# Kernel optimization log

Hardware: AMD Instinct MI355X
Metric: run time of the kernel (lower is better)

## Reference

```python
import jax, jax.numpy as jnp
import numpy as np

T, B, E, H = 64, 64, 128, 256
N_ITEMS, N_DATA = 50000, 20000
EPS = 1e-8


def setup_inputs() -> dict:
    key = jax.random.key(0)
    ks = jax.random.split(key, 20)
    lengths = jnp.sort(jax.random.randint(ks[0], (B,), 1, T + 1))[::-1]
    lengths = lengths.at[0].set(T)  # pack_padded_sequence expects max length first
    x = jax.random.randint(ks[1], (T, B), 1, N_ITEMS)
    tmask = jnp.arange(T)[:, None] < lengths[None, :]
    x = jnp.where(tmask, x, 0)  # padding index 0
    s = 0.05
    emb_table = (jax.random.normal(ks[2], (N_ITEMS, E)) * s).at[0].set(0.0)  # padding_idx=0
    data_embeddings = jax.random.normal(ks[3], (N_DATA, E)) * s
    return {
        'x': x, 'lengths': lengths,
        'emb_table': emb_table, 'data_embeddings': data_embeddings,
        'W_ih': jax.random.normal(ks[4], (4 * H, E)) * s,
        'W_hh': jax.random.normal(ks[5], (4 * H, H)) * s,
        'b_ih': jax.random.normal(ks[6], (4 * H,)) * s,
        'b_hh': jax.random.normal(ks[7], (4 * H,)) * s,
        'Wq': jax.random.normal(ks[8], (H, H)) * s, 'bq': jax.random.normal(ks[9], (H,)) * s,
        'Wk': jax.random.normal(ks[10], (H, H)) * s, 'bk': jax.random.normal(ks[11], (H,)) * s,
        'Wv': jax.random.normal(ks[12], (H, H)) * s, 'bv': jax.random.normal(ks[13], (H,)) * s,
        'W_out': jax.random.normal(ks[14], (E, H)) * s, 'b_out': jax.random.normal(ks[15], (E,)) * s,
    }


def _forward(x, lengths, emb_table, data_embeddings, W_ih, W_hh, b_ih, b_hh,
             Wq, bq, Wk, bk, Wv, bv, W_out, b_out):
    t_len, b_sz = x.shape
    e_dim = emb_table.shape[1]
    h_dim = W_hh.shape[1]

    embs0 = emb_table[x]  # (T, B, E); dropout is identity in eval mode
    initial_embs = jax.lax.stop_gradient(embs0)  # .clone().detach() in original

    # PositionalEncoding: original slices by x.size(1) == batch dim (faithful quirk)
    pos = jnp.arange(b_sz, dtype=jnp.float32)[:, None]
    div = jnp.exp(jnp.arange(0, e_dim, 2, dtype=jnp.float32) * (-jnp.log(10000.0) / e_dim))
    enc = jnp.stack([jnp.sin(pos * div), jnp.cos(pos * div)], axis=-1).reshape(b_sz, e_dim)
    embs = embs0 + enc[None, :, :]  # broadcast over time

    # single-layer LSTM over time (gate order i, f, g, o)
    def step(carry, x_t):
        h, c = carry
        gates = x_t @ W_ih.T + h @ W_hh.T + (b_ih + b_hh)  # (B, 4H)
        i, f, g, o = jnp.split(gates, 4, axis=-1)
        c = jax.nn.sigmoid(f) * c + jax.nn.sigmoid(i) * jnp.tanh(g)
        h = jax.nn.sigmoid(o) * jnp.tanh(c)
        return (h, c), h

    h0 = jnp.zeros((b_sz, h_dim), embs.dtype)
    (_, _), lstm_out = jax.lax.scan(step, (h0, h0), embs)  # (T, B, H)

    # pack/pad round-trip zeroes outputs past each length (LSTM is causal)
    tmask = jnp.arange(t_len)[:, None] < lengths[None, :]  # (T, B)
    lstm_out = lstm_out * tmask[:, :, None]
    lstm_out = lstm_out.transpose(1, 0, 2)  # (B, T, H)

    padding_mask = jnp.sum(lstm_out, axis=-1) != 0  # (B, T)

    q = lstm_out @ Wq.T + bq
    k = lstm_out @ Wk.T + bk
    v = lstm_out @ Wv.T + bv
    score = jnp.einsum('bth,bsh->bts', q, k) / jnp.sqrt(jnp.float32(h_dim))
    score = jnp.where(padding_mask[:, None, :], score, -jnp.inf)
    attn = jax.nn.softmax(score, axis=2)
    weighted = jnp.einsum('bts,bsh->bth', attn, v)  # (B, T, H)
    attn_output = jnp.mean(weighted, axis=1) @ W_out.T + b_out  # (B, E)

    # kNN: fused normalize + matmul + argmin + gather over all T at once
    qn = initial_embs / jnp.clip(jnp.linalg.norm(initial_embs, axis=-1, keepdims=True), EPS)
    dn = data_embeddings / jnp.clip(jnp.linalg.norm(data_embeddings, axis=-1, keepdims=True), EPS)
    sims = jnp.einsum('tbe,ne->tbn', qn, dn)  # (T, B, N_DATA)
    idx = jnp.argmax(sims, axis=-1)  # argmin of (1 - sim)
    closest = jnp.mean(data_embeddings[idx], axis=0)  # (B, E)

    attn_output = attn_output * closest
    return attn_output @ emb_table.T  # (B, n_items)


def reference(x, lengths, emb_table, data_embeddings, W_ih, W_hh, b_ih, b_hh,
              Wq, bq, Wk, bk, Wv, bv, W_out, b_out):
    return _forward(x, lengths, emb_table, data_embeddings, W_ih, W_hh, b_ih, b_hh,
                    Wq, bq, Wk, bk, Wv, bv, W_out, b_out)
```

## Files before the change

kernel.cpp:

```cpp
#include <hip/hip_runtime.h>

typedef unsigned int uint;
typedef unsigned short ushort;
typedef unsigned long long u64;

#define NITEMS 50000
#define NDATA  20000
#define BLKCAP 4096u
#define OVCAP  65536u

#define OFF_LSTMOUT   0x0000000ULL
#define OFF_HX        0x0400000ULL
#define OFF_HXM       0x0440000ULL
#define OFF_PACKED    0x0480000ULL
#define OFF_PACKED2   0x0488000ULL
#define OFF_HITCNTS   0x0490000ULL
#define OFF_OHITCNT   0x0490800ULL
#define MEMSET_BYTES  0x0491000ULL
#define OFF_QMARGIN   0x0491000ULL
#define OFF_XW        0x05A0000ULL
#define OFF_QKV       0x15A0000ULL
#define OFF_HITBUF    OFF_QKV
#define OFF_WIHT      0x21A0000ULL
#define OFF_WQKVT     0x2220000ULL
#define OFF_BIASIH    0x22E0000ULL
#define OFF_BQKV      0x22E1000ULL
#define OFF_DNSCALE   0x22E2000ULL
#define OFF_CLOSEST   0x22F6000ULL
#define OFF_AV        0x22FE000ULL
#define OFF_DEMB16    0x2306000ULL
#define OFF_A16       0x27E8000ULL
#define OFF_OVF       0x28E8000ULL

__device__ __forceinline__ ushort f2bf(float f) {
  union { float f; uint u; } v; v.f = f;
  uint u = v.u;
  return (ushort)((u + 0x7FFFu + ((u >> 16) & 1u)) >> 16);
}
__device__ __forceinline__ uint fkey(float f) {
  union { float f; uint u; } v; v.f = f;
  return (v.u & 0x80000000u) ? ~v.u : (v.u | 0x80000000u);
}
__device__ __forceinline__ u64 shfl_xor_u64(u64 v, int off) {
  uint lo = (uint)v, hi = (uint)(v >> 32);
  lo = (uint)__shfl_xor((int)lo, off);
  hi = (uint)__shfl_xor((int)hi, off);
  return ((u64)hi << 32) | (u64)lo;
}

typedef __attribute__((ext_vector_type(8))) short short8;
typedef __attribute__((ext_vector_type(4))) float floatx4;

#define R32(M) M(0) M(1) M(2) M(3) M(4) M(5) M(6) M(7) M(8) M(9) M(10) M(11) \
  M(12) M(13) M(14) M(15) M(16) M(17) M(18) M(19) M(20) M(21) M(22) M(23) \
  M(24) M(25) M(26) M(27) M(28) M(29) M(30) M(31)

#define HIX(j) ((j) + (((j) >> 7) << 2))

#define LBAR() do { \
  __builtin_amdgcn_sched_barrier(0); \
  asm volatile("s_waitcnt lgkmcnt(0)" ::: "memory"); \
  __builtin_amdgcn_s_barrier(); \
  __builtin_amdgcn_sched_barrier(0); \
} while (0)

__global__ __launch_bounds__(256) void prep_kernel(
    const int* __restrict__ x,
    const float* __restrict__ emb, const float* __restrict__ demb,
    const float* __restrict__ W_ih,
    const float* __restrict__ Wq, const float* __restrict__ Wk, const float* __restrict__ Wv,
    const float* __restrict__ b_ih, const float* __restrict__ b_hh,
    const float* __restrict__ bq, const float* __restrict__ bk, const float* __restrict__ bv,
    float* __restrict__ dnscale, ushort* __restrict__ demb16, ushort* __restrict__ a16,
    float* __restrict__ wiht, float* __restrict__ wqkvt,
    float* __restrict__ biasih, float* __restrict__ bqkv,
    float* __restrict__ qmargin, u64* __restrict__ packed2)
{
  int blk = blockIdx.x, tid = threadIdx.x;
  if (blk < 5000) {
    int row = blk * 4 + (tid >> 6);
    int lane = tid & 63;
    float2 d = *(const float2*)(demb + (size_t)row * 128 + lane * 2);
    float s = d.x * d.x + d.y * d.y;
    for (int off = 32; off; off >>= 1) s += __shfl_xor(s, off);
    if (lane == 0) dnscale[row] = 1.0f / fmaxf(sqrtf(s), 1e-8f);
  } else if (blk < 6250) {
    size_t base = ((size_t)(blk - 5000) * 256 + tid) * 8;
    float4 f1 = *(const float4*)(demb + base);
    float4 f2 = *(const float4*)(demb + base + 4);
    uint4 o;
    o.x = (uint)f2bf(f1.x) | ((uint)f2bf(f1.y) << 16);
    o.y = (uint)f2bf(f1.z) | ((uint)f2bf(f1.w) << 16);
    o.z = (uint)f2bf(f2.x) | ((uint)f2bf(f2.y) << 16);
    o.w = (uint)f2bf(f2.z) | ((uint)f2bf(f2.w) << 16);
    *(uint4*)(demb16 + base) = o;
  } else if (blk < 6506) {
    int idx = (blk - 6250) * 256 + tid;
    int m = idx >> 4, seg = idx & 15;
    const float* src = emb + (size_t)x[m] * 128 + seg * 8;
    float4 f1 = *(const float4*)(src);
    float4 f2 = *(const float4*)(src + 4);
    uint4 o;
    o.x = (uint)f2bf(f1.x) | ((uint)f2bf(f1.y) << 16);
    o.y = (uint)f2bf(f1.z) | ((uint)f2bf(f1.w) << 16);
    o.z = (uint)f2bf(f2.x) | ((uint)f2bf(f2.y) << 16);
    o.w = (uint)f2bf(f2.z) | ((uint)f2bf(f2.w) << 16);
    *(uint4*)(a16 + (size_t)m * 128 + seg * 8) = o;
  } else if (blk < 7018) {
    int f = (blk - 6506) * 256 + tid;
    int r = f >> 7, e = f & 127;
    wiht[e * 1024 + r] = W_ih[f];
  } else if (blk < 7786) {
    int f = (blk - 7018) * 256 + tid;
    int w = f >> 16; int rem = f & 65535;
    int r = rem >> 8, e = rem & 255;
    const float* src = (w == 0) ? Wq : (w == 1) ? Wk : Wv;
    wqkvt[e * 768 + w * 256 + r] = src[rem];
  } else if (blk < 7790) {
    int idx = (blk - 7786) * 256 + tid;
    if (idx < 1024) biasih[idx] = b_ih[idx] + b_hh[idx];
  } else if (blk < 7793) {
    int idx = (blk - 7790) * 256 + tid;
    if (idx < 768) {
      int w = idx >> 8; int r = idx & 255;
      const float* src = (w == 0) ? bq : (w == 1) ? bk : bv;
      bqkv[idx] = src[r];
    }
  } else {
    int row = (blk - 7793) * 4 + (tid >> 6);
    int lane = tid & 63;
    float2 d = *(const float2*)(emb + (size_t)x[row] * 128 + lane * 2);
    float s = d.x * d.x + d.y * d.y;
    for (int off = 32; off; off >>= 1) s += __shfl_xor(s, off);
    if (lane == 0) {
      if (s == 0.f) {
        qmargin[row] = -1e30f;
        packed2[row] = ((u64)fkey(0.0f) << 32) | 0xFFFFFFFFull;
      } else {
        qmargin[row] = 0.017f * sqrtf(s) + 1e-5f;
      }
    }
  }
}

__global__ __launch_bounds__(256) void xw_kernel(
    const int* __restrict__ x, const float* __restrict__ emb,
    const float* __restrict__ wiht, const float* __restrict__ biasih,
    float* __restrict__ xW)
{
  __shared__ __align__(16) float At[128 * 16];
  int blk = blockIdx.x, tid = threadIdx.x;
  int m0 = blk * 16;
  for (int c = 0; c < 8; ++c) {
    int idx = c * 256 + tid;
    int mm = idx >> 7, e = idx & 127;
    int m = m0 + mm;
    int bcol = m & 63;
    int xv = x[m];
    float val = emb[(size_t)xv * 128 + e];
    int j = e >> 1;
    float arg = (float)bcol * __expf((float)j * -0.14391157f);
    val += (e & 1) ? cosf(arg) : sinf(arg);
    At[e * 16 + mm] = val;
  }
  __syncthreads();
  int quad = tid >> 6, l = tid & 63;
  for (int rp = 0; rp < 4; ++rp) {
    int r = rp * 256 + l * 4;
    float acc[4][4] = {};
    for (int e = 0; e < 128; ++e) {
      float4 wv4 = *(const float4*)(wiht + e * 1024 + r);
      float4 av4 = *(const float4*)(At + e * 16 + quad * 4);
      float am[4] = {av4.x, av4.y, av4.z, av4.w};
      float wr4[4] = {wv4.x, wv4.y, wv4.z, wv4.w};
      #pragma unroll
      for (int mi = 0; mi < 4; ++mi)
        #pragma unroll
        for (int ri = 0; ri < 4; ++ri)
          acc[mi][ri] += am[mi] * wr4[ri];
    }
    float4 bv4 = *(const float4*)(biasih + r);
    #pragma unroll
    for (int mi = 0; mi < 4; ++mi) {
      size_t m = (size_t)(m0 + quad * 4 + mi);
      float4 o;
      o.x = acc[mi][0] + bv4.x; o.y = acc[mi][1] + bv4.y;
      o.z = acc[mi][2] + bv4.z; o.w = acc[mi][3] + bv4.w;
      *(float4*)(xW + m * 1024 + r) = o;
    }
  }
}

__global__ __launch_bounds__(256) void knn_kernel(
    const ushort* __restrict__ a16, const ushort* __restrict__ demb16,
    const float* __restrict__ dnscale, const float* __restrict__ qmargin,
    u64* __restrict__ packed, uint* __restrict__ hitcnts, uint* __restrict__ ohitcnt,
    uint* __restrict__ hitbuf, uint* __restrict__ ovbuf,
    const int* __restrict__ x, const float* __restrict__ emb,
    const float* __restrict__ demb, u64* __restrict__ packed2)
{
  __shared__ __align__(16) ushort b_sh[2][64 * 144];
  __shared__ uint lcnt;
  int blk = blockIdx.x, tid = threadIdx.x;
  int chunk = blk & 15, mt = blk >> 4;
  int wv = tid >> 6, lane = tid & 63;
  int col = lane & 15, quad = lane >> 4;
  int M0 = mt * 128;
  if (tid == 0) lcnt = 0;
  short8 afrag[2][4];
  #pragma unroll
  for (int s = 0; s < 2; ++s) {
    int mrow = M0 + s * 64 + wv * 16 + col;
    #pragma unroll
    for (int kf = 0; kf < 4; ++kf)
      afrag[s][kf] = *(const short8*)(a16 + (size_t)mrow * 128 + kf * 32 + quad * 8);
  }
  float best[2][4] = {{-1e30f,-1e30f,-1e30f,-1e30f},{-1e30f,-1e30f,-1e30f,-1e30f}};
  int bidx[2][4] = {};
  int nbase = chunk * 1250, nend = nbase + 1250;
  const int niter = 20;
  int srow = tid >> 4, sseg = tid & 15;
  uint4 stg[4]; float scr[4];

  #pragma unroll
  for (int p = 0; p < 4; ++p) {
    int n = nbase + p * 16 + srow;
    uint4 v = {0u,0u,0u,0u};
    if (n < nend) v = *(const uint4*)(demb16 + (size_t)n * 128 + sseg * 8);
    stg[p] = v;
  }
  #pragma unroll
  for (int ns = 0; ns < 4; ++ns) {
    int n = nbase + ns * 16 + col;
    scr[ns] = (n < nend) ? dnscale[n] : 0.f;
  }
  for (int it = 0; it < niter; ++it) {
    int n0 = nbase + it * 64;
    ushort* bsh = b_sh[it & 1];
    #pragma unroll
    for (int p = 0; p < 4; ++p)
      *(uint4*)(&bsh[(p * 16 + srow) * 144 + sseg * 8]) = stg[p];
    float mysc[4] = {scr[0], scr[1], scr[2], scr[3]};
    __syncthreads();
    if (it + 1 < niter) {
      int nb = n0 + 64;
      #pragma unroll
      for (int p = 0; p < 4; ++p) {
        int n = nb + p * 16 + srow;
        uint4 v = {0u,0u,0u,0u};
        if (n < nend) v = *(const uint4*)(demb16 + (size_t)n * 128 + sseg * 8);
        stg[p] = v;
      }
      #pragma unroll
      for (int ns = 0; ns < 4; ++ns) {
        int n = nb + ns * 16 + col;
        scr[ns] = (n < nend) ? dnscale[n] : 0.f;
      }
    }
    #pragma unroll
    for (int ns = 0; ns < 4; ++ns) {
      short8 bfr[4];
      #pragma unroll
      for (int kf = 0; kf < 4; ++kf)
        bfr[kf] = *(const short8*)(&bsh[(ns * 16 + col) * 144 + kf * 32 + quad * 8]);
      int n = n0 + ns * 16 + col;
      float sc = mysc[ns];
      bool valid = (n < nend);
      #pragma unroll
      for (int s = 0; s < 2; ++s) {
        floatx4 acc = {0.f, 0.f, 0.f, 0.f};
        #pragma unroll
        for (int kf = 0; kf < 4; ++kf)
          acc = __builtin_amdgcn_mfma_f32_16x16x32_bf16(afrag[s][kf], bfr[kf], acc, 0, 0, 0);
        #pragma unroll
        for (int r = 0; r < 4; ++r) {
          float sim = acc[r] * sc;
          if (valid && sim > best[s][r]) { best[s][r] = sim; bidx[s][r] = n; }
        }
      }
    }
  }
  float thr[2][4];
  #pragma unroll
  for (int s = 0; s < 2; ++s)
    #pragma unroll
    for (int r = 0; r < 4; ++r) {
      u64 p = ((u64)fkey(best[s][r]) << 32) | (u64)(0xFFFFFFFFu - (uint)bidx[s][r]);
      #pragma unroll
      for (int off = 1; off < 16; off <<= 1) {
        u64 o = shfl_xor_u64(p, off);
        if (o > p) p = o;
      }
      int m = M0 + s * 64 + wv * 16 + quad * 4 + r;
      union { uint u; float f; } bu;
      uint k = (uint)(p >> 32);
      bu.u = (k & 0x80000000u) ? (k & 0x7FFFFFFFu) : ~k;
      thr[s][r] = bu.f - qmargin[m];
      if (col == 0)
        atomicMax((unsigned long long*)&packed[m], (unsigned long long)p);
    }
  __syncthreads();

  uint* myregion = hitbuf + (size_t)blk * BLKCAP;
  uint* ovregion = ovbuf;
  #pragma unroll
  for (int p = 0; p < 4; ++p) {
    int n = nbase + p * 16 + srow;
    uint4 v = {0u,0u,0u,0u};
    if (n < nend) v = *(const uint4*)(demb16 + (size_t)n * 128 + sseg * 8);
    stg[p] = v;
  }
  #pragma unroll
  for (int ns = 0; ns < 4; ++ns) {
    int n = nbase + ns * 16 + col;
    scr[ns] = (n < nend) ? dnscale[n] : 0.f;
  }
  for (int it = 0; it < niter; ++it) {
    int n0 = nbase + it * 64;
    ushort* bsh = b_sh[it & 1];
    #pragma unroll
    for (int p = 0; p < 4; ++p)
      *(uint4*)(&bsh[(p * 16 + srow) * 144 + sseg * 8]) = stg[p];
    float mysc[4] = {scr[0], scr[1], scr[2], scr[3]};
    __syncthreads();
    if (it + 1 < niter) {
      int nb = n0 + 64;
      #pragma unroll
      for (int p = 0; p < 4; ++p) {
        int n = nb + p * 16 + srow;
        uint4 v = {0u,0u,0u,0u};
        if (n < nend) v = *(const uint4*)(demb16 + (size_t)n * 128 + sseg * 8);
        stg[p] = v;
      }
      #pragma unroll
      for (int ns = 0; ns < 4; ++ns) {
        int n = nb + ns * 16 + col;
        scr[ns] = (n < nend) ? dnscale[n] : 0.f;
      }
    }
    #pragma unroll
    for (int ns = 0; ns < 4; ++ns) {
      short8 bfr[4];
      #pragma unroll
      for (int kf = 0; kf < 4; ++kf)
        bfr[kf] = *(const short8*)(&bsh[(ns * 16 + col) * 144 + kf * 32 + quad * 8]);
      int n = n0 + ns * 16 + col;
      float sc = mysc[ns];
      bool valid = (n < nend);
      #pragma unroll
      for (int s = 0; s < 2; ++s) {
        floatx4 acc = {0.f, 0.f, 0.f, 0.f};
        #pragma unroll
        for (int kf = 0; kf < 4; ++kf)
          acc = __builtin_amdgcn_mfma_f32_16x16x32_bf16(afrag[s][kf], bfr[kf], acc, 0, 0, 0);
        #pragma unroll
        for (int r = 0; r < 4; ++r) {
          float sim = acc[r] * sc;
          bool hit = valid && (sim >= thr[s][r]);
          u64 mask = __ballot(hit);
          if (mask) {
            uint lcntv = (uint)__popcll(mask);
            int leader = __ffsll((unsigned long long)mask) - 1;
            uint base = 0;
            if (lane == leader) base = atomicAdd(&lcnt, lcntv);
            base = (uint)__shfl((int)base, leader);
            if (hit) {
              uint pos = base + (uint)__popcll(mask & ((1ull << lane) - 1ull));
              uint mm = (uint)(M0 + s * 64 + wv * 16 + quad * 4 + r);
              uint rec = (mm << 15) | (uint)n;
              if (pos < BLKCAP) {
                myregion[pos] = rec;
              } else {
                uint op = atomicAdd(ohitcnt, 1u);
                if (op < OVCAP) ovregion[op] = rec;
              }
            }
          }
        }
      }
    }
  }
  __syncthreads();
  if (tid == 0) hitcnts[blk] = lcnt;
  uint rcnt = lcnt; if (rcnt > BLKCAP) rcnt = BLKCAP;
  for (uint h = tid; h < rcnt; h += 256) {
    uint rec = myregion[h];
    uint m = rec >> 15, n = rec & 0x7FFFu;
    if (m >= 4096 || n >= NDATA) continue;
    const float* qr = emb + (size_t)x[m] * 128;
    const float* dr = demb + (size_t)n * 128;
    double p = 0.0;
    #pragma unroll 8
    for (int e = 0; e < 128; e += 2) {
      float2 qv = *(const float2*)(qr + e);
      float2 dv = *(const float2*)(dr + e);
      p += (double)qv.x * (double)dv.x + (double)qv.y * (double)dv.y;
    }
    float sx = (float)(p * (double)dnscale[n]);
    u64 key = ((u64)fkey(sx) << 32) | (u64)(0xFFFFFFFFu - n);
    atomicMax((unsigned long long*)&packed2[m], (unsigned long long)key);
  }
}

__global__ __launch_bounds__(512, 2) void lstm_kernel(
    const int* __restrict__ lengths, const float* __restrict__ Whh,
    const float* __restrict__ xW, float* __restrict__ lstm_out,
    u64* __restrict__ hx, u64* __restrict__ hxm)
{
  __shared__ __align__(16) float h_sh[264];
  __shared__ float part_sh[256];
  int blk = blockIdx.x, tid = threadIdx.x;
  int b = blk & 63, q = blk >> 6;
  int row_local = tid >> 1, half = tid & 1;
  int gate = row_local >> 6, jloc = row_local & 63;
  int grow = gate * 256 + q * 64 + jloc;
  const float4* wp4 = (const float4*)(Whh + (size_t)grow * 256 + half * 128);
#define WDECL(i) float4 tt##i = wp4[i]; \
  float w##i##x = tt##i.x, w##i##y = tt##i.y, w##i##z = tt##i.z, w##i##w = tt##i.w;
  R32(WDECL)
#define WPIN(i) asm volatile("" : "+v"(w##i##x), "+v"(w##i##y), "+v"(w##i##z), "+v"(w##i##w));
  R32(WPIN)
  int len = lengths[b];
  if (tid < 256) h_sh[HIX(tid)] = 0.f;
  float cval = 0.f;
  int prm = tid - 320;
  int jr = (prm < q * 64) ? prm : prm + 64;
  bool fast_ok = true;
  int j1 = q * 64 + (tid - 64);
  float xw0 = 0.f, xw1 = 0.f, xw2 = 0.f, xw3 = 0.f;
  if (tid < 64) {
    const float* xwrow = xW + ((size_t)0 * 64 + b) * 1024 + q * 64 + tid;
    xw0 = xwrow[0]; xw1 = xwrow[256]; xw2 = xwrow[512]; xw3 = xwrow[768];
  }
  __syncthreads();
  for (int t = 0; t < len; ++t) {
    float nx0 = 0.f, nx1 = 0.f, nx2 = 0.f, nx3 = 0.f;
    if (tid < 64 && t + 1 < len) {
      const float* xwrow = xW + ((size_t)(t + 1) * 64 + b) * 1024 + q * 64 + tid;
      nx0 = xwrow[0]; nx1 = xwrow[256]; nx2 = xwrow[512]; nx3 = xwrow[768];
    }
    float hprev = 0.f;
    if (tid >= 64 && tid < 128 && t > 0) hprev = h_sh[HIX(j1)];
    const float4* h4 = (const float4*)(h_sh + half * 132);
    float a[4] = {0.f, 0.f, 0.f, 0.f};
#define WACC(i) { float4 hv_ = h4[i]; \
    a[(i) & 3] += w##i##x * hv_.x + w##i##y * hv_.y + w##i##z * hv_.z + w##i##w * hv_.w; }
    R32(WACC)
    float acc = (a[0] + a[2]) + (a[1] + a[3]);
    acc += __shfl_xor(acc, 1);
    if (!half) part_sh[row_local] = acc;
    LBAR();
    if (tid < 64) {
      float gi = part_sh[tid]       + xw0;
      float gf = part_sh[64 + tid]  + xw1;
      float gg = part_sh[128 + tid] + xw2;
      float go = part_sh[192 + tid] + xw3;
      float ii = 1.f / (1.f + __expf(-gi));
      float ff = 1.f / (1.f + __expf(-gf));
      float oo = 1.f / (1.f + __expf(-go));
      float tg = 1.f - 2.f / (1.f + __expf(2.f * gg));
      cval = ff * cval + ii * tg;
      float tc = 1.f - 2.f / (1.f + __expf(2.f * cval));
      float hv = oo * tc;
      int j = q * 64 + tid;
      union { float f; uint u; } cu; cu.f = hv;
      u64 pk = ((u64)cu.u << 32) | (u64)(uint)(t + 1);
      size_t slot = ((size_t)((t + 1) & 1) * 64 + b) * 256 + j;
      __builtin_amdgcn_sched_barrier(0);
      asm volatile("s_waitcnt vmcnt(4)" ::: "memory");
      asm volatile("global_store_dwordx2 %0, %1, off"
                   :: "v"(hxm + slot), "v"(pk) : "memory");
      __hip_atomic_store(hx + slot, pk, __ATOMIC_RELAXED, __HIP_MEMORY_SCOPE_AGENT);
      h_sh[HIX(j)] = hv;
      xw0 = nx0; xw1 = nx1; xw2 = nx2; xw3 = nx3;
    } else if (tid < 128) {
      if (t > 0) lstm_out[((size_t)b * 64 + (t - 1)) * 256 + j1] = hprev;
    } else if (tid >= 320 && t + 1 < len) {
      size_t slot = ((size_t)((t + 1) & 1) * 64 + b) * 256 + jr;
      uint want = (uint)(t + 1);
      u64 v = 0;
      bool got = false;
      if (fast_ok) {
        const u64* ms = hxm + slot;
        for (int tries = 0; tries < 32; ++tries) {
          asm volatile("global_load_dwordx2 %0, %1, off sc0\n\t"
                       "s_waitcnt vmcnt(0)"
                       : "=&v"(v) : "v"(ms) : "memory");
          if ((uint)v == want) { got = true; break; }
        }
        if (!got && t > 0) fast_ok = false;
      }
      if (!got) {
        const u64* as = hx + slot;
        int guard = 0;
        while (true) {
          v = __hip_atomic_load(as, __ATOMIC_RELAXED, __HIP_MEMORY_SCOPE_AGENT);
          if ((uint)v == want || ++guard > (1 << 24)) break;
        }
      }
      union { uint u; float f; } cv; cv.u = (uint)(v >> 32);
      h_sh[HIX(jr)] = cv.f;
    }
    LBAR();
  }
  if (tid >= 64 && tid < 128) {
    float hl = h_sh[HIX(j1)];
    lstm_out[((size_t)b * 64 + (len - 1)) * 256 + j1] = hl;
  }
}

__global__ __launch_bounds__(256) void fused_post_kernel(
    const float* __restrict__ lstm_out, const float* __restrict__ wqkvt,
    const float* __restrict__ bqkv, float* __restrict__ qkv,
    const u64* __restrict__ packed, const uint* __restrict__ ohitcnt,
    const uint* __restrict__ ovbuf, const int* __restrict__ x,
    const float* __restrict__ emb, const float* __restrict__ demb,
    const float* __restrict__ dnscale, u64* __restrict__ packed2)
{
  __shared__ __align__(16) float At[256 * 16];
  int blk = blockIdx.x, tid = threadIdx.x;
  if (blk < 256) {
    int m0 = blk * 16;
    for (int c = 0; c < 16; ++c)
      At[tid * 16 + c] = lstm_out[((size_t)m0 + c) * 256 + tid];
    __syncthreads();
    int quad = tid >> 6, l = tid & 63;
    for (int rp = 0; rp < 3; ++rp) {
      int r = rp * 256 + l * 4;
      float acc[4][4] = {};
      for (int e = 0; e < 256; ++e) {
        float4 wv4 = *(const float4*)(wqkvt + (size_t)e * 768 + r);
        float4 av4 = *(const float4*)(At + e * 16 + quad * 4);
        float am[4] = {av4.x, av4.y, av4.z, av4.w};
        float wr4[4] = {wv4.x, wv4.y, wv4.z, wv4.w};
        #pragma unroll
        for (int mi = 0; mi < 4; ++mi)
          #pragma unroll
          for (int ri = 0; ri < 4; ++ri)
            acc[mi][ri] += am[mi] * wr4[ri];
      }
      float4 bv4 = *(const float4*)(bqkv + r);
      #pragma unroll
      for (int mi = 0; mi < 4; ++mi) {
        size_t m = (size_t)(m0 + quad * 4 + mi);
        float4 o;
        o.x = acc[mi][0] + bv4.x; o.y = acc[mi][1] + bv4.y;
        o.z = acc[mi][2] + bv4.z; o.w = acc[mi][3] + bv4.w;
        *(float4*)(qkv + m * 768 + r) = o;
      }
    }
    return;
  }
  if (blk < 272) {
    uint m = (uint)(blk - 256) * 256 + tid;
    uint n = 0xFFFFFFFFu - (uint)(packed[m] & 0xFFFFFFFFull);
    if (n < NDATA) {
      const float* qr = emb + (size_t)x[m] * 128;
      const float* dr = demb + (size_t)n * 128;
      double p = 0.0;
      #pragma unroll 8
      for (int e = 0; e < 128; e += 2) {
        float2 qv = *(const float2*)(qr + e);
        float2 dv = *(const float2*)(dr + e);
        p += (double)qv.x * (double)dv.x + (double)qv.y * (double)dv.y;
      }
      float sx = (float)(p * (double)dnscale[n]);
      u64 key = ((u64)fkey(sx) << 32) | (u64)(0xFFFFFFFFu - n);
      atomicMax((unsigned long long*)&packed2[m], (unsigned long long)key);
    }
    return;
  }
  uint cnt = *ohitcnt; if (cnt > OVCAP) cnt = OVCAP;
  for (uint h = (uint)(blk - 272) * 256 + tid; h < cnt; h += 16 * 256) {
    uint rec = ovbuf[h];
    uint m = rec >> 15, n = rec & 0x7FFFu;
    if (m >= 4096 || n >= NDATA) continue;
    const float* qr = emb + (size_t)x[m] * 128;
    const float* dr = demb + (size_t)n * 128;
    double p = 0.0;
    #pragma unroll 8
    for (int e = 0; e < 128; e += 2) {
      float2 qv = *(const float2*)(qr + e);
      float2 dv = *(const float2*)(dr + e);
      p += (double)qv.x * (double)dv.x + (double)qv.y * (double)dv.y;
    }
    float sx = (float)(p * (double)dnscale[n]);
    u64 key = ((u64)fkey(sx) << 32) | (u64)(0xFFFFFFFFu - n);
    atomicMax((unsigned long long*)&packed2[m], (unsigned long long)key);
  }
}

__global__ __launch_bounds__(128) void closest_kernel(
    const u64* __restrict__ packed2, const float* __restrict__ demb,
    float* __restrict__ closest)
{
  int b = blockIdx.x, tid = threadIdx.x;
  float s = 0.f;
  for (int t = 0; t < 64; ++t) {
    uint low = (uint)(packed2[t * 64 + b] & 0xFFFFFFFFull);
    uint n = 0xFFFFFFFFu - low;
    if (n >= NDATA) n = 0;
    s += demb[(size_t)n * 128 + tid];
  }
  closest[b * 128 + tid] = s * (1.0f / 64.0f);
}

__global__ __launch_bounds__(256) void attn_kernel(
    const float* __restrict__ qkv, const int* __restrict__ lengths,
    const float* __restrict__ closest, const float* __restrict__ W_out,
    const float* __restrict__ b_out, float* __restrict__ av)
{
  __shared__ float k_sh[64 * 257];
  __shared__ __align__(16) float q_sh[4 * 256];
  __shared__ float wpart[4 * 64];
  __shared__ float wtot[64];
  __shared__ float out_sh[256];
  int b = blockIdx.x, tid = threadIdx.x;
  int wv = tid >> 6, lane = tid & 63;
  int len = lengths[b];
  for (int s = 0; s < 64; ++s)
    k_sh[s * 257 + tid] = qkv[((size_t)b * 64 + s) * 768 + 256 + tid];
  wpart[tid] = 0.f;
  for (int tq = 0; tq < 16; ++tq) {
    __syncthreads();
    #pragma unroll
    for (int c = 0; c < 4; ++c)
      q_sh[c * 256 + tid] = qkv[((size_t)b * 64 + tq * 4 + c) * 768 + tid];
    __syncthreads();
    const float* krow = k_sh + lane * 257;
    const float* qrow = q_sh + wv * 256;
    float sc = 0.f;
    #pragma unroll 8
    for (int h = 0; h < 256; ++h)
      sc += qrow[h] * krow[h];
    sc *= 0.0625f;
    bool vs = (lane < len);
    float scm = vs ? sc : -1e30f;
    float mx = scm;
    for (int off = 32; off; off >>= 1) mx = fmaxf(mx, __shfl_xor(mx, off));
    float e = vs ? __expf(sc - mx) : 0.f;
    float sum = e;
    for (int off = 32; off; off >>= 1) sum += __shfl_xor(sum, off);
    wpart[wv * 64 + lane] += e / sum;
  }
  __syncthreads();
  if (tid < 64)
    wtot[tid] = (wpart[tid] + wpart[64 + tid] + wpart[128 + tid] + wpart[192 + tid]) * (1.0f / 64.0f);
  __syncthreads();
  {
    float acc = 0.f;
    for (int s = 0; s < 64; ++s)
      acc += wtot[s] * qkv[((size_t)b * 64 + s) * 768 + 512 + tid];
    out_sh[tid] = acc;
  }
  __syncthreads();
  if (tid < 128) {
    const float4* wr = (const float4*)(W_out + (size_t)tid * 256);
    float p = b_out[tid];
    #pragma unroll
    for (int c = 0; c < 64; ++c) {
      float4 u = wr[c];
      p += out_sh[c * 4 + 0] * u.x + out_sh[c * 4 + 1] * u.y
         + out_sh[c * 4 + 2] * u.z + out_sh[c * 4 + 3] * u.w;
    }
    av[tid * 64 + b] = p * closest[b * 128 + tid];
  }
}

__global__ __launch_bounds__(256) void final_kernel(
    const float* __restrict__ emb, const float* __restrict__ av,
    float* __restrict__ out)
{
  int i = blockIdx.x * 256 + threadIdx.x;
  if (i >= NITEMS) return;
  const float4* row = (const float4*)(emb + (size_t)i * 128);
  float acc[64];
  #pragma unroll
  for (int bb = 0; bb < 64; ++bb) acc[bb] = 0.f;
  for (int e4 = 0; e4 < 32; ++e4) {
    float4 u = row[e4];
    float wvv[4] = {u.x, u.y, u.z, u.w};
    const float* ab = av + e4 * 4 * 64;
    #pragma unroll
    for (int j = 0; j < 4; ++j) {
      #pragma unroll
      for (int bb = 0; bb < 64; ++bb)
        acc[bb] += wvv[j] * ab[j * 64 + bb];
    }
  }
  #pragma unroll
  for (int bb = 0; bb < 64; ++bb)
    out[(size_t)bb * NITEMS + i] = acc[bb];
}

extern "C" void kernel_launch(void* const* d_in, const int* in_sizes, int n_in,
                              void* d_out, int out_size, void* d_ws, size_t ws_size,
                              hipStream_t stream)
{
  const int*   x       = (const int*)d_in[0];
  const int*   lengths = (const int*)d_in[1];
  const float* emb     = (const float*)d_in[2];
  const float* demb    = (const float*)d_in[3];
  const float* W_ih    = (const float*)d_in[4];
  const float* W_hh    = (const float*)d_in[5];
  const float* b_ih    = (const float*)d_in[6];
  const float* b_hh    = (const float*)d_in[7];
  const float* Wq      = (const float*)d_in[8];
  const float* bq      = (const float*)d_in[9];
  const float* Wk      = (const float*)d_in[10];
  const float* bk      = (const float*)d_in[11];
  const float* Wv      = (const float*)d_in[12];
  const float* bv      = (const float*)d_in[13];
  const float* W_out   = (const float*)d_in[14];
  const float* b_out   = (const float*)d_in[15];

  char* ws = (char*)d_ws;
  float*  lstm_out = (float*)(ws + OFF_LSTMOUT);
  u64*    hx       = (u64*)(ws + OFF_HX);
  u64*    hxm      = (u64*)(ws + OFF_HXM);
  u64*    packed   = (u64*)(ws + OFF_PACKED);
  u64*    packed2  = (u64*)(ws + OFF_PACKED2);
  uint*   hitcnts  = (uint*)(ws + OFF_HITCNTS);
  uint*   ohitcnt  = (uint*)(ws + OFF_OHITCNT);
  float*  qmargin  = (float*)(ws + OFF_QMARGIN);
  uint*   hitbuf   = (uint*)(ws + OFF_HITBUF);
  uint*   ovbuf    = (uint*)(ws + OFF_OVF);
  float*  xW       = (float*)(ws + OFF_XW);
  float*  qkv      = (float*)(ws + OFF_QKV);
  float*  wiht     = (float*)(ws + OFF_WIHT);
  float*  wqkvt    = (float*)(ws + OFF_WQKVT);
  float*  biasih   = (float*)(ws + OFF_BIASIH);
  float*  bqkv     = (float*)(ws + OFF_BQKV);
  float*  dnscale  = (float*)(ws + OFF_DNSCALE);
  float*  closest  = (float*)(ws + OFF_CLOSEST);
  float*  av       = (float*)(ws + OFF_AV);
  ushort* demb16   = (ushort*)(ws + OFF_DEMB16);
  ushort* a16      = (ushort*)(ws + OFF_A16);

  hipMemsetAsync(d_ws, 0, (size_t)MEMSET_BYTES, stream);

  hipLaunchKernelGGL(prep_kernel, dim3(8817), dim3(256), 0, stream,
                     x, emb, demb, W_ih, Wq, Wk, Wv, b_ih, b_hh, bq, bk, bv,
                     dnscale, demb16, a16, wiht, wqkvt, biasih, bqkv,
                     qmargin, packed2);
  hipLaunchKernelGGL(xw_kernel, dim3(256), dim3(256), 0, stream,
                     x, emb, wiht, biasih, xW);
  hipLaunchKernelGGL(knn_kernel, dim3(512), dim3(256), 0, stream,
                     a16, demb16, dnscale, qmargin, packed, hitcnts, ohitcnt,
                     hitbuf, ovbuf, x, emb, demb, packed2);
  hipLaunchKernelGGL(lstm_kernel, dim3(256), dim3(512), 0, stream,
                     lengths, W_hh, xW, lstm_out, hx, hxm);
  hipLaunchKernelGGL(fused_post_kernel, dim3(288), dim3(256), 0, stream,
                     lstm_out, wqkvt, bqkv, qkv, packed, ohitcnt, ovbuf,
                     x, emb, demb, dnscale, packed2);
  hipLaunchKernelGGL(closest_kernel, dim3(64), dim3(128), 0, stream,
                     packed2, demb, closest);
  hipLaunchKernelGGL(attn_kernel, dim3(64), dim3(256), 0, stream,
                     qkv, lengths, closest, W_out, b_out, av);
  hipLaunchKernelGGL(final_kernel, dim3(196), dim3(256), 0, stream,
                     emb, av, (float*)d_out);
}
```

Baseline: 584.8 us.

## Merge LSTM and kNN into one launch and fold closest into attention

Combines the latency-bound LSTM recurrence (256 blocks) and the kNN MFMA search (now 512-thread blocks, one 64-row slice per wave group) into a single 768-block launch. The kNN work can then run on compute units the serial LSTM leaves idle. The separate closest_kernel is also removed and its gather-mean is computed inside attn_kernel, saving one launch and a round trip through global memory. The risks are that the LSTM blocks rely on cross-block spin-waiting, so they must all be resident at once, and that kNN blocks competing with them for CUs may slow the critical recurrence.

```diff
diff --git a/kernel.cpp b/kernel.cpp
--- a/kernel.cpp
+++ b/kernel.cpp
@@ -26,7 +26,6 @@
 #define OFF_BIASIH    0x22E0000ULL
 #define OFF_BQKV      0x22E1000ULL
 #define OFF_DNSCALE   0x22E2000ULL
-#define OFF_CLOSEST   0x22F6000ULL
 #define OFF_AV        0x22FE000ULL
 #define OFF_DEMB16    0x2306000ULL
 #define OFF_A16       0x27E8000ULL
@@ -191,7 +190,10 @@
   }
 }
 
-__global__ __launch_bounds__(256) void knn_kernel(
+__global__ __launch_bounds__(512, 2) void lstm_knn_kernel(
+    const int* __restrict__ lengths, const float* __restrict__ Whh,
+    const float* __restrict__ xW, float* __restrict__ lstm_out,
+    u64* __restrict__ hx, u64* __restrict__ hxm,
     const ushort* __restrict__ a16, const ushort* __restrict__ demb16,
     const float* __restrict__ dnscale, const float* __restrict__ qmargin,
     u64* __restrict__ packed, uint* __restrict__ hitcnts, uint* __restrict__ ohitcnt,
@@ -199,32 +201,139 @@
     const int* __restrict__ x, const float* __restrict__ emb,
     const float* __restrict__ demb, u64* __restrict__ packed2)
 {
+  __shared__ __align__(16) float h_sh[264];
+  __shared__ float part_sh[256];
   __shared__ __align__(16) ushort b_sh[2][64 * 144];
   __shared__ uint lcnt;
-  int blk = blockIdx.x, tid = threadIdx.x;
-  int chunk = blk & 15, mt = blk >> 4;
-  int wv = tid >> 6, lane = tid & 63;
+  int tid = threadIdx.x;
+
+  if (blockIdx.x < 256) {
+    int blk = blockIdx.x;
+    int b = blk & 63, q = blk >> 6;
+    int row_local = tid >> 1, half = tid & 1;
+    int gate = row_local >> 6, jloc = row_local & 63;
+    int grow = gate * 256 + q * 64 + jloc;
+    const float4* wp4 = (const float4*)(Whh + (size_t)grow * 256 + half * 128);
+#define WDECL(i) float4 tt##i = wp4[i]; \
+  float w##i##x = tt##i.x, w##i##y = tt##i.y, w##i##z = tt##i.z, w##i##w = tt##i.w;
+    R32(WDECL)
+#define WPIN(i) asm volatile("" : "+v"(w##i##x), "+v"(w##i##y), "+v"(w##i##z), "+v"(w##i##w));
+    R32(WPIN)
+    int len = lengths[b];
+    if (tid < 256) h_sh[HIX(tid)] = 0.f;
+    float cval = 0.f;
+    int prm = tid - 320;
+    int jr = (prm < q * 64) ? prm : prm + 64;
+    bool fast_ok = true;
+    int j1 = q * 64 + (tid - 64);
+    float xw0 = 0.f, xw1 = 0.f, xw2 = 0.f, xw3 = 0.f;
+    if (tid < 64) {
+      const float* xwrow = xW + ((size_t)0 * 64 + b) * 1024 + q * 64 + tid;
+      xw0 = xwrow[0]; xw1 = xwrow[256]; xw2 = xwrow[512]; xw3 = xwrow[768];
+    }
+    __syncthreads();
+    for (int t = 0; t < len; ++t) {
+      float nx0 = 0.f, nx1 = 0.f, nx2 = 0.f, nx3 = 0.f;
+      if (tid < 64 && t + 1 < len) {
+        const float* xwrow = xW + ((size_t)(t + 1) * 64 + b) * 1024 + q * 64 + tid;
+        nx0 = xwrow[0]; nx1 = xwrow[256]; nx2 = xwrow[512]; nx3 = xwrow[768];
+      }
+      float hprev = 0.f;
+      if (tid >= 64 && tid < 128 && t > 0) hprev = h_sh[HIX(j1)];
+      const float4* h4 = (const float4*)(h_sh + half * 132);
+      float a[4] = {0.f, 0.f, 0.f, 0.f};
+#define WACC(i) { float4 hv_ = h4[i]; \
+    a[(i) & 3] += w##i##x * hv_.x + w##i##y * hv_.y + w##i##z * hv_.z + w##i##w * hv_.w; }
+      R32(WACC)
+      float acc = (a[0] + a[2]) + (a[1] + a[3]);
+      acc += __shfl_xor(acc, 1);
+      if (!half) part_sh[row_local] = acc;
+      LBAR();
+      if (tid < 64) {
+        float gi = part_sh[tid]       + xw0;
+        float gf = part_sh[64 + tid]  + xw1;
+        float gg = part_sh[128 + tid] + xw2;
+        float go = part_sh[192 + tid] + xw3;
+        float ii = 1.f / (1.f + __expf(-gi));
+        float ff = 1.f / (1.f + __expf(-gf));
+        float oo = 1.f / (1.f + __expf(-go));
+        float tg = 1.f - 2.f / (1.f + __expf(2.f * gg));
+        cval = ff * cval + ii * tg;
+        float tc = 1.f - 2.f / (1.f + __expf(2.f * cval));
+        float hv = oo * tc;
+        int j = q * 64 + tid;
+        union { float f; uint u; } cu; cu.f = hv;
+        u64 pk = ((u64)cu.u << 32) | (u64)(uint)(t + 1);
+        size_t slot = ((size_t)((t + 1) & 1) * 64 + b) * 256 + j;
+        __builtin_amdgcn_sched_barrier(0);
+        asm volatile("s_waitcnt vmcnt(4)" ::: "memory");
+        asm volatile("global_store_dwordx2 %0, %1, off"
+                     :: "v"(hxm + slot), "v"(pk) : "memory");
+        __hip_atomic_store(hx + slot, pk, __ATOMIC_RELAXED, __HIP_MEMORY_SCOPE_AGENT);
+        h_sh[HIX(j)] = hv;
+        xw0 = nx0; xw1 = nx1; xw2 = nx2; xw3 = nx3;
+      } else if (tid < 128) {
+        if (t > 0) lstm_out[((size_t)b * 64 + (t - 1)) * 256 + j1] = hprev;
+      } else if (tid >= 320 && t + 1 < len) {
+        size_t slot = ((size_t)((t + 1) & 1) * 64 + b) * 256 + jr;
+        uint want = (uint)(t + 1);
+        u64 v = 0;
+        bool got = false;
+        if (fast_ok) {
+          const u64* ms = hxm + slot;
+          for (int tries = 0; tries < 32; ++tries) {
+            asm volatile("global_load_dwordx2 %0, %1, off sc0\n\t"
+                         "s_waitcnt vmcnt(0)"
+                         : "=&v"(v) : "v"(ms) : "memory");
+            if ((uint)v == want) { got = true; break; }
+          }
+          if (!got && t > 0) fast_ok = false;
+        }
+        if (!got) {
+          const u64* as = hx + slot;
+          int guard = 0;
+          while (true) {
+            v = __hip_atomic_load(as, __ATOMIC_RELAXED, __HIP_MEMORY_SCOPE_AGENT);
+            if ((uint)v == want || ++guard > (1 << 24)) break;
+          }
+        }
+        union { uint u; float f; } cv; cv.u = (uint)(v >> 32);
+        h_sh[HIX(jr)] = cv.f;
+      }
+      LBAR();
+    }
+    if (tid >= 64 && tid < 128) {
+      float hl = h_sh[HIX(j1)];
+      lstm_out[((size_t)b * 64 + (len - 1)) * 256 + j1] = hl;
+    }
+    return;
+  }
+
+  int kb = blockIdx.x - 256;
+  int chunk = kb & 15, mt = kb >> 4;
+  int w8 = tid >> 6;
+  int s = w8 >> 2, wv2 = w8 & 3;
+  int lane = tid & 63;
   int col = lane & 15, quad = lane >> 4;
   int M0 = mt * 128;
   if (tid == 0) lcnt = 0;
-  short8 afrag[2][4];
-  #pragma unroll
-  for (int s = 0; s < 2; ++s) {
-    int mrow = M0 + s * 64 + wv * 16 + col;
+  short8 afrag[4];
+  {
+    int mrow = M0 + s * 64 + wv2 * 16 + col;
     #pragma unroll
     for (int kf = 0; kf < 4; ++kf)
-      afrag[s][kf] = *(const short8*)(a16 + (size_t)mrow * 128 + kf * 32 + quad * 8);
-  }
-  float best[2][4] = {{-1e30f,-1e30f,-1e30f,-1e30f},{-1e30f,-1e30f,-1e30f,-1e30f}};
-  int bidx[2][4] = {};
+      afrag[kf] = *(const short8*)(a16 + (size_t)mrow * 128 + kf * 32 + quad * 8);
+  }
+  float best[4] = {-1e30f, -1e30f, -1e30f, -1e30f};
+  int bidx[4] = {};
   int nbase = chunk * 1250, nend = nbase + 1250;
   const int niter = 20;
   int srow = tid >> 4, sseg = tid & 15;
-  uint4 stg[4]; float scr[4];
+  uint4 stg[2]; float scr[4];
 
   #pragma unroll
-  for (int p = 0; p < 4; ++p) {
-    int n = nbase + p * 16 + srow;
+  for (int p = 0; p < 2; ++p) {
+    int n = nbase + p * 32 + srow;
     uint4 v = {0u,0u,0u,0u};
     if (n < nend) v = *(const uint4*)(demb16 + (size_t)n * 128 + sseg * 8);
     stg[p] = v;
@@ -238,15 +347,15 @@
     int n0 = nbase + it * 64;
     ushort* bsh = b_sh[it & 1];
     #pragma unroll
-    for (int p = 0; p < 4; ++p)
-      *(uint4*)(&bsh[(p * 16 + srow) * 144 + sseg * 8]) = stg[p];
+    for (int p = 0; p < 2; ++p)
+      *(uint4*)(&bsh[(p * 32 + srow) * 144 + sseg * 8]) = stg[p];
     float mysc[4] = {scr[0], scr[1], scr[2], scr[3]};
     __syncthreads();
     if (it + 1 < niter) {
       int nb = n0 + 64;
       #pragma unroll
-      for (int p = 0; p < 4; ++p) {
-        int n = nb + p * 16 + srow;
+      for (int p = 0; p < 2; ++p) {
+        int n = nb + p * 32 + srow;
         uint4 v = {0u,0u,0u,0u};
         if (n < nend) v = *(const uint4*)(demb16 + (size_t)n * 128 + sseg * 8);
         stg[p] = v;
@@ -266,46 +375,41 @@
       int n = n0 + ns * 16 + col;
       float sc = mysc[ns];
       bool valid = (n < nend);
-      #pragma unroll
-      for (int s = 0; s < 2; ++s) {
-        floatx4 acc = {0.f, 0.f, 0.f, 0.f};
-        #pragma unroll
-        for (int kf = 0; kf < 4; ++kf)
-          acc = __builtin_amdgcn_mfma_f32_16x16x32_bf16(afrag[s][kf], bfr[kf], acc, 0, 0, 0);
-        #pragma unroll
-        for (int r = 0; r < 4; ++r) {
-          float sim = acc[r] * sc;
-          if (valid && sim > best[s][r]) { best[s][r] = sim; bidx[s][r] = n; }
-        }
-      }
-    }
-  }
-  float thr[2][4];
+      floatx4 acc = {0.f, 0.f, 0.f, 0.f};
+      #pragma unroll
+      for (int kf = 0; kf < 4; ++kf)
+        acc = __builtin_amdgcn_mfma_f32_16x16x32_bf16(afrag[kf], bfr[kf], acc, 0, 0, 0);
+      #pragma unroll
+      for (int r = 0; r < 4; ++r) {
+        float sim = acc[r] * sc;
+        if (valid && sim > best[r]) { best[r] = sim; bidx[r] = n; }
+      }
+    }
+  }
+  float thr[4];
   #pragma unroll
-  for (int s = 0; s < 2; ++s)
-    #pragma unroll
-    for (int r = 0; r < 4; ++r) {
-      u64 p = ((u64)fkey(best[s][r]) << 32) | (u64)(0xFFFFFFFFu - (uint)bidx[s][r]);
-      #pragma unroll
-      for (int off = 1; off < 16; off <<= 1) {
-        u64 o = shfl_xor_u64(p, off);
-        if (o > p) p = o;
-      }
-      int m = M0 + s * 64 + wv * 16 + quad * 4 + r;
-      union { uint u; float f; } bu;
-      uint k = (uint)(p >> 32);
-      bu.u = (k & 0x80000000u) ? (k & 0x7FFFFFFFu) : ~k;
-      thr[s][r] = bu.f - qmargin[m];
-      if (col == 0)
-        atomicMax((unsigned long long*)&packed[m], (unsigned long long)p);
-    }
+  for (int r = 0; r < 4; ++r) {
+    u64 p = ((u64)fkey(best[r]) << 32) | (u64)(0xFFFFFFFFu - (uint)bidx[r]);
+    #pragma unroll
+    for (int off = 1; off < 16; off <<= 1) {
+      u64 o = shfl_xor_u64(p, off);
+      if (o > p) p = o;
+    }
+    int m = M0 + s * 64 + wv2 * 16 + quad * 4 + r;
+    union { uint u; float f; } bu;
+    uint k = (uint)(p >> 32);
+    bu.u = (k & 0x80000000u) ? (k & 0x7FFFFFFFu) : ~k;
+    thr[r] = bu.f - qmargin[m];
+    if (col == 0)
+      atomicMax((unsigned long long*)&packed[m], (unsigned long long)p);
+  }
   __syncthreads();
 
-  uint* myregion = hitbuf + (size_t)blk * BLKCAP;
+  uint* myregion = hitbuf + (size_t)kb * BLKCAP;
   uint* ovregion = ovbuf;
   #pragma unroll
-  for (int p = 0; p < 4; ++p) {
-    int n = nbase + p * 16 + srow;
+  for (int p = 0; p < 2; ++p) {
+    int n = nbase + p * 32 + srow;
     uint4 v = {0u,0u,0u,0u};
     if (n < nend) v = *(const uint4*)(demb16 + (size_t)n * 128 + sseg * 8);
     stg[p] = v;
@@ -319,15 +423,15 @@
     int n0 = nbase + it * 64;
     ushort* bsh = b_sh[it & 1];
     #pragma unroll
-    for (int p = 0; p < 4; ++p)
-      *(uint4*)(&bsh[(p * 16 + srow) * 144 + sseg * 8]) = stg[p];
+    for (int p = 0; p < 2; ++p)
+      *(uint4*)(&bsh[(p * 32 + srow) * 144 + sseg * 8]) = stg[p];
     float mysc[4] = {scr[0], scr[1], scr[2], scr[3]};
     __syncthreads();
     if (it + 1 < niter) {
       int nb = n0 + 64;
       #pragma unroll
-      for (int p = 0; p < 4; ++p) {
-        int n = nb + p * 16 + srow;
+      for (int p = 0; p < 2; ++p) {
+        int n = nb + p * 32 + srow;
         uint4 v = {0u,0u,0u,0u};
         if (n < nend) v = *(const uint4*)(demb16 + (size_t)n * 128 + sseg * 8);
         stg[p] = v;
@@ -347,33 +451,30 @@
       int n = n0 + ns * 16 + col;
       float sc = mysc[ns];
       bool valid = (n < nend);
-      #pragma unroll
-      for (int s = 0; s < 2; ++s) {
-        floatx4 acc = {0.f, 0.f, 0.f, 0.f};
-        #pragma unroll
-        for (int kf = 0; kf < 4; ++kf)
-          acc = __builtin_amdgcn_mfma_f32_16x16x32_bf16(afrag[s][kf], bfr[kf], acc, 0, 0, 0);
-        #pragma unroll
-        for (int r = 0; r < 4; ++r) {
-          float sim = acc[r] * sc;
-          bool hit = valid && (sim >= thr[s][r]);
-          u64 mask = __ballot(hit);
-          if (mask) {
-            uint lcntv = (uint)__popcll(mask);
-            int leader = __ffsll((unsigned long long)mask) - 1;
-            uint base = 0;
-            if (lane == leader) base = atomicAdd(&lcnt, lcntv);
-            base = (uint)__shfl((int)base, leader);
-            if (hit) {
-              uint pos = base + (uint)__popcll(mask & ((1ull << lane) - 1ull));
-              uint mm = (uint)(M0 + s * 64 + wv * 16 + quad * 4 + r);
-              uint rec = (mm << 15) | (uint)n;
-              if (pos < BLKCAP) {
-                myregion[pos] = rec;
-              } else {
-                uint op = atomicAdd(ohitcnt, 1u);
-                if (op < OVCAP) ovregion[op] = rec;
-              }
+      floatx4 acc = {0.f, 0.f, 0.f, 0.f};
+      #pragma unroll
+      for (int kf = 0; kf < 4; ++kf)
+        acc = __builtin_amdgcn_mfma_f32_16x16x32_bf16(afrag[kf], bfr[kf], acc, 0, 0, 0);
+      #pragma unroll
+      for (int r = 0; r < 4; ++r) {
+        float sim = acc[r] * sc;
+        bool hit = valid && (sim >= thr[r]);
+        u64 mask = __ballot(hit);
+        if (mask) {
+          uint lcntv = (uint)__popcll(mask);
+          int leader = __ffsll((unsigned long long)mask) - 1;
+          uint base = 0;
+          if (lane == leader) base = atomicAdd(&lcnt, lcntv);
+          base = (uint)__shfl((int)base, leader);
+          if (hit) {
+            uint pos = base + (uint)__popcll(mask & ((1ull << lane) - 1ull));
+            uint mm = (uint)(M0 + s * 64 + wv2 * 16 + quad * 4 + r);
+            uint rec = (mm << 15) | (uint)n;
+            if (pos < BLKCAP) {
+              myregion[pos] = rec;
+            } else {
+              uint op = atomicAdd(ohitcnt, 1u);
+              if (op < OVCAP) ovregion[op] = rec;
             }
           }
         }
@@ -381,9 +482,9 @@
     }
   }
   __syncthreads();
-  if (tid == 0) hitcnts[blk] = lcnt;
+  if (tid == 0) hitcnts[kb] = lcnt;
   uint rcnt = lcnt; if (rcnt > BLKCAP) rcnt = BLKCAP;
-  for (uint h = tid; h < rcnt; h += 256) {
+  for (uint h = tid; h < rcnt; h += 512) {
     uint rec = myregion[h];
     uint m = rec >> 15, n = rec & 0x7FFFu;
     if (m >= 4096 || n >= NDATA) continue;
@@ -399,113 +500,6 @@
     float sx = (float)(p * (double)dnscale[n]);
     u64 key = ((u64)fkey(sx) << 32) | (u64)(0xFFFFFFFFu - n);
     atomicMax((unsigned long long*)&packed2[m], (unsigned long long)key);
-  }
-}
-
-__global__ __launch_bounds__(512, 2) void lstm_kernel(
-    const int* __restrict__ lengths, const float* __restrict__ Whh,
-    const float* __restrict__ xW, float* __restrict__ lstm_out,
-    u64* __restrict__ hx, u64* __restrict__ hxm)
-{
-  __shared__ __align__(16) float h_sh[264];
-  __shared__ float part_sh[256];
-  int blk = blockIdx.x, tid = threadIdx.x;
-  int b = blk & 63, q = blk >> 6;
-  int row_local = tid >> 1, half = tid & 1;
-  int gate = row_local >> 6, jloc = row_local & 63;
-  int grow = gate * 256 + q * 64 + jloc;
-  const float4* wp4 = (const float4*)(Whh + (size_t)grow * 256 + half * 128);
-#define WDECL(i) float4 tt##i = wp4[i]; \
-  float w##i##x = tt##i.x, w##i##y = tt##i.y, w##i##z = tt##i.z, w##i##w = tt##i.w;
-  R32(WDECL)
-#define WPIN(i) asm volatile("" : "+v"(w##i##x), "+v"(w##i##y), "+v"(w##i##z), "+v"(w##i##w));
-  R32(WPIN)
-  int len = lengths[b];
-  if (tid < 256) h_sh[HIX(tid)] = 0.f;
-  float cval = 0.f;
-  int prm = tid - 320;
-  int jr = (prm < q * 64) ? prm : prm + 64;
-  bool fast_ok = true;
-  int j1 = q * 64 + (tid - 64);
-  float xw0 = 0.f, xw1 = 0.f, xw2 = 0.f, xw3 = 0.f;
-  if (tid < 64) {
-    const float* xwrow = xW + ((size_t)0 * 64 + b) * 1024 + q * 64 + tid;
-    xw0 = xwrow[0]; xw1 = xwrow[256]; xw2 = xwrow[512]; xw3 = xwrow[768];
-  }
-  __syncthreads();
-  for (int t = 0; t < len; ++t) {
-    float nx0 = 0.f, nx1 = 0.f, nx2 = 0.f, nx3 = 0.f;
-    if (tid < 64 && t + 1 < len) {
-      const float* xwrow = xW + ((size_t)(t + 1) * 64 + b) * 1024 + q * 64 + tid;
-      nx0 = xwrow[0]; nx1 = xwrow[256]; nx2 = xwrow[512]; nx3 = xwrow[768];
-    }
-    float hprev = 0.f;
-    if (tid >= 64 && tid < 128 && t > 0) hprev = h_sh[HIX(j1)];
-    const float4* h4 = (const float4*)(h_sh + half * 132);
-    float a[4] = {0.f, 0.f, 0.f, 0.f};
-#define WACC(i) { float4 hv_ = h4[i]; \
-    a[(i) & 3] += w##i##x * hv_.x + w##i##y * hv_.y + w##i##z * hv_.z + w##i##w * hv_.w; }
-    R32(WACC)
-    float acc = (a[0] + a[2]) + (a[1] + a[3]);
-    acc += __shfl_xor(acc, 1);
-    if (!half) part_sh[row_local] = acc;
-    LBAR();
-    if (tid < 64) {
-      float gi = part_sh[tid]       + xw0;
-      float gf = part_sh[64 + tid]  + xw1;
-      float gg = part_sh[128 + tid] + xw2;
-      float go = part_sh[192 + tid] + xw3;
-      float ii = 1.f / (1.f + __expf(-gi));
-      float ff = 1.f / (1.f + __expf(-gf));
-      float oo = 1.f / (1.f + __expf(-go));
-      float tg = 1.f - 2.f / (1.f + __expf(2.f * gg));
-      cval = ff * cval + ii * tg;
-      float tc = 1.f - 2.f / (1.f + __expf(2.f * cval));
-      float hv = oo * tc;
-      int j = q * 64 + tid;
-      union { float f; uint u; } cu; cu.f = hv;
-      u64 pk = ((u64)cu.u << 32) | (u64)(uint)(t + 1);
-      size_t slot = ((size_t)((t + 1) & 1) * 64 + b) * 256 + j;
-      __builtin_amdgcn_sched_barrier(0);
-      asm volatile("s_waitcnt vmcnt(4)" ::: "memory");
-      asm volatile("global_store_dwordx2 %0, %1, off"
-                   :: "v"(hxm + slot), "v"(pk) : "memory");
-      __hip_atomic_store(hx + slot, pk, __ATOMIC_RELAXED, __HIP_MEMORY_SCOPE_AGENT);
-      h_sh[HIX(j)] = hv;
-      xw0 = nx0; xw1 = nx1; xw2 = nx2; xw3 = nx3;
-    } else if (tid < 128) {
-      if (t > 0) lstm_out[((size_t)b * 64 + (t - 1)) * 256 + j1] = hprev;
-    } else if (tid >= 320 && t + 1 < len) {
-      size_t slot = ((size_t)((t + 1) & 1) * 64 + b) * 256 + jr;
-      uint want = (uint)(t + 1);
-      u64 v = 0;
-      bool got = false;
-      if (fast_ok) {
-        const u64* ms = hxm + slot;
-        for (int tries = 0; tries < 32; ++tries) {
-          asm volatile("global_load_dwordx2 %0, %1, off sc0\n\t"
-                       "s_waitcnt vmcnt(0)"
-                       : "=&v"(v) : "v"(ms) : "memory");
-          if ((uint)v == want) { got = true; break; }
-        }
-        if (!got && t > 0) fast_ok = false;
-      }
-      if (!got) {
-        const u64* as = hx + slot;
-        int guard = 0;
-        while (true) {
-          v = __hip_atomic_load(as, __ATOMIC_RELAXED, __HIP_MEMORY_SCOPE_AGENT);
-          if ((uint)v == want || ++guard > (1 << 24)) break;
-        }
-      }
-      union { uint u; float f; } cv; cv.u = (uint)(v >> 32);
-      h_sh[HIX(jr)] = cv.f;
-    }
-    LBAR();
-  }
-  if (tid >= 64 && tid < 128) {
-    float hl = h_sh[HIX(j1)];
-    lstm_out[((size_t)b * 64 + (len - 1)) * 256 + j1] = hl;
   }
 }
 
@@ -590,25 +584,11 @@
   }
 }
 
-__global__ __launch_bounds__(128) void closest_kernel(
-    const u64* __restrict__ packed2, const float* __restrict__ demb,
-    float* __restrict__ closest)
-{
-  int b = blockIdx.x, tid = threadIdx.x;
-  float s = 0.f;
-  for (int t = 0; t < 64; ++t) {
-    uint low = (uint)(packed2[t * 64 + b] & 0xFFFFFFFFull);
-    uint n = 0xFFFFFFFFu - low;
-    if (n >= NDATA) n = 0;
-    s += demb[(size_t)n * 128 + tid];
-  }
-  closest[b * 128 + tid] = s * (1.0f / 64.0f);
-}
-
 __global__ __launch_bounds__(256) void attn_kernel(
     const float* __restrict__ qkv, const int* __restrict__ lengths,
-    const float* __restrict__ closest, const float* __restrict__ W_out,
-    const float* __restrict__ b_out, float* __restrict__ av)
+    const u64* __restrict__ packed2, const float* __restrict__ demb,
+    const float* __restrict__ W_out, const float* __restrict__ b_out,
+    float* __restrict__ av)
 {
   __shared__ float k_sh[64 * 257];
   __shared__ __align__(16) float q_sh[4 * 256];
@@ -620,6 +600,17 @@
   int len = lengths[b];
   for (int s = 0; s < 64; ++s)
     k_sh[s * 257 + tid] = qkv[((size_t)b * 64 + s) * 768 + 256 + tid];
+  float clv = 0.f;
+  if (tid < 128) {
+    float sum = 0.f;
+    for (int t = 0; t < 64; ++t) {
+      uint low = (uint)(packed2[t * 64 + b] & 0xFFFFFFFFull);
+      uint n = 0xFFFFFFFFu - low;
+      if (n >= NDATA) n = 0;
+      sum += demb[(size_t)n * 128 + tid];
+    }
+    clv = sum * (1.0f / 64.0f);
+  }
   wpart[tid] = 0.f;
   for (int tq = 0; tq < 16; ++tq) {
     __syncthreads();
@@ -663,7 +654,7 @@
       p += out_sh[c * 4 + 0] * u.x + out_sh[c * 4 + 1] * u.y
          + out_sh[c * 4 + 2] * u.z + out_sh[c * 4 + 3] * u.w;
     }
-    av[tid * 64 + b] = p * closest[b * 128 + tid];
+    av[tid * 64 + b] = p * clv;
   }
 }
 
@@ -732,7 +723,6 @@
   float*  biasih   = (float*)(ws + OFF_BIASIH);
   float*  bqkv     = (float*)(ws + OFF_BQKV);
   float*  dnscale  = (float*)(ws + OFF_DNSCALE);
-  float*  closest  = (float*)(ws + OFF_CLOSEST);
   float*  av       = (float*)(ws + OFF_AV);
   ushort* demb16   = (ushort*)(ws + OFF_DEMB16);
   ushort* a16      = (ushort*)(ws + OFF_A16);
@@ -745,18 +735,15 @@
                      qmargin, packed2);
   hipLaunchKernelGGL(xw_kernel, dim3(256), dim3(256), 0, stream,
                      x, emb, wiht, biasih, xW);
-  hipLaunchKernelGGL(knn_kernel, dim3(512), dim3(256), 0, stream,
+  hipLaunchKernelGGL(lstm_knn_kernel, dim3(768), dim3(512), 0, stream,
+                     lengths, W_hh, xW, lstm_out, hx, hxm,
                      a16, demb16, dnscale, qmargin, packed, hitcnts, ohitcnt,
                      hitbuf, ovbuf, x, emb, demb, packed2);
-  hipLaunchKernelGGL(lstm_kernel, dim3(256), dim3(512), 0, stream,
-                     lengths, W_hh, xW, lstm_out, hx, hxm);
   hipLaunchKernelGGL(fused_post_kernel, dim3(288), dim3(256), 0, stream,
                      lstm_out, wqkvt, bqkv, qkv, packed, ohitcnt, ovbuf,
                      x, emb, demb, dnscale, packed2);
-  hipLaunchKernelGGL(closest_kernel, dim3(64), dim3(128), 0, stream,
-                     packed2, demb, closest);
   hipLaunchKernelGGL(attn_kernel, dim3(64), dim3(256), 0, stream,
-                     qkv, lengths, closest, W_out, b_out, av);
+                     qkv, lengths, packed2, demb, W_out, b_out, av);
   hipLaunchKernelGGL(final_kernel, dim3(196), dim3(256), 0, stream,
                      emb, av, (float*)d_out);
 }
```

Result: no change. 587.2 us (median of 2 runs) (+0.4%).
